# Kernel tuning notes

Hardware: AMD Instinct MI355X
Metric: run time of the kernel (lower is better)

## Reference

```python
import jax, jax.numpy as jnp
import numpy as np

LOG_2PI = float(np.log(2.0 * np.pi))


def setup_inputs() -> dict:
    key = jax.random.key(0)
    ks = jax.random.split(key, 6)
    T, K, Dx, Dy = 131072, 32, 16, 16
    X = jax.random.normal(ks[0], (T, Dx), dtype=jnp.float32)
    Y = jax.random.normal(ks[1], (T, Dy), dtype=jnp.float32)
    init_logits = jnp.zeros((K,), dtype=jnp.float32)
    W = jax.random.normal(ks[2], (K, K, Dx), dtype=jnp.float32) * 0.1
    b = jax.random.normal(ks[3], (K, K), dtype=jnp.float32) * 0.1
    mu = jax.random.normal(ks[4], (K, Dy), dtype=jnp.float32) * 0.1
    raw_log_var = jnp.zeros((K, Dy), dtype=jnp.float32)
    return {"X": X, "Y": Y, "init_logits": init_logits, "W": W, "b": b,
            "mu": mu, "raw_log_var": raw_log_var}


def _hmm_loglik(X, Y, init_logits, W, b, mu, raw_log_var):
    D = Y.shape[-1]
    # Emission log-probs for all t, k at once: [T, K]
    log_var = jnp.clip(raw_log_var, -6.0, 6.0)            # [K, Dy]
    diff = Y[:, None, :] - mu[None, :, :]                 # [T, K, Dy]
    quad = jnp.sum(diff * diff * jnp.exp(-log_var), axis=-1)  # [T, K]
    log_em = -0.5 * (D * LOG_2PI + jnp.sum(log_var, axis=-1) + quad)  # [T, K]
    # Time-varying log transition matrices, rows (axis i->j, softmax over j): [T, K, K]
    logits = b[None, :, :] + jnp.einsum('ijd,td->tij', W, X)
    log_A = jax.nn.log_softmax(logits, axis=2)
    # Forward recursion in log domain via scan.
    alpha0 = jax.nn.log_softmax(init_logits) + log_em[0]  # [K]
    def step(alpha, inp):
        lA, le = inp  # [K, K], [K]
        alpha = le + jax.scipy.special.logsumexp(alpha[:, None] + lA, axis=0)
        return alpha, None
    alphaT, _ = jax.lax.scan(step, alpha0, (log_A[1:], log_em[1:]))
    return jax.scipy.special.logsumexp(alphaT)


def reference(X, Y, init_logits, W, b, mu, raw_log_var):
    return _hmm_loglik(X, Y, init_logits, W, b, mu, raw_log_var)
```

## Files before the change

kernel.cpp:

```cpp
#include <hip/hip_runtime.h>

typedef float  f32x16 __attribute__((ext_vector_type(16)));
typedef float  f32x2  __attribute__((ext_vector_type(2)));
typedef short  short8 __attribute__((ext_vector_type(8)));
typedef unsigned short u16;
typedef unsigned int   u32;

#define LOG2PI_F 1.8378770664093453f

__device__ __forceinline__ u16 f2bf(float f) {
  u32 u = __builtin_bit_cast(u32, f);
  u32 r = (u + 0x7FFFu + ((u >> 16) & 1u)) >> 16;
  return (u16)r;
}

__global__ __launch_bounds__(256) void emis_kernel(
    const float* __restrict__ Y, const float* __restrict__ mu,
    const float* __restrict__ rlv, int T,
    float* __restrict__ E, float* __restrict__ Spart)
{
  int j  = threadIdx.x & 31;
  int ts = threadIdx.x >> 5;

  float muv[16], iv[16];
  float slv = 0.f;
  const float4* mp = (const float4*)(mu  + (size_t)j * 16);
  const float4* rp = (const float4*)(rlv + (size_t)j * 16);
#pragma unroll
  for (int q = 0; q < 4; ++q) {
    float4 m4 = mp[q], r4 = rp[q];
    float mm[4] = {m4.x, m4.y, m4.z, m4.w};
    float rr[4] = {r4.x, r4.y, r4.z, r4.w};
#pragma unroll
    for (int e = 0; e < 4; ++e) {
      float lv = fminf(fmaxf(rr[e], -6.f), 6.f);
      muv[4*q+e] = mm[e];
      iv[4*q+e]  = __expf(-lv);
      slv += lv;
    }
  }
  float base_c = 16.f * LOG2PI_F + slv;

  float sacc = 0.f;
  for (int p2 = 0; p2 < 8; ++p2) {
    int t = blockIdx.x * 64 + p2 * 8 + ts;
    if (t < T) {
      float quad = 0.f;
      const float4* yp = (const float4*)(Y + (size_t)t * 16);
#pragma unroll
      for (int q = 0; q < 4; ++q) {
        float4 y4 = yp[q];
        float yy[4] = {y4.x, y4.y, y4.z, y4.w};
#pragma unroll
        for (int e = 0; e < 4; ++e) {
          float d = yy[e] - muv[4*q+e];
          quad = fmaf(d * d, iv[4*q+e], quad);
        }
      }
      float lem = -0.5f * (base_c + quad);
      float mx = lem;
#pragma unroll
      for (int m = 16; m >= 1; m >>= 1) mx = fmaxf(mx, __shfl_xor(mx, m, 32));
      E[(size_t)t * 32 + j] = __expf(lem - mx);
      if (j == 0) sacc += mx;
    }
  }
  __shared__ float sred[8];
  if (j == 0) sred[ts] = sacc;
  __syncthreads();
  if (threadIdx.x == 0) {
    float s = 0.f;
#pragma unroll
    for (int k = 0; k < 8; ++k) s += sred[k];
    Spart[blockIdx.x] = s;
  }
}

__global__ __launch_bounds__(256) void prep_kernel(
    const float* __restrict__ W, const float* __restrict__ b,
    u16* __restrict__ Wfrag, float* __restrict__ bprime)
{
  const float INVLN2 = 1.4426950408889634f;
  int idx = blockIdx.x * 256 + threadIdx.x;
  if (idx < 16384) {
    int i = idx >> 9, rem = idx & 511, l = rem >> 3, e = rem & 7;
    int j = l & 31, h = l >> 5;
    Wfrag[idx] = f2bf(W[i * 512 + j * 16 + h * 8 + e] * INVLN2);
  }
  if (idx < 1024) bprime[idx] = b[idx] * INVLN2;
}

__device__ __forceinline__ void acc_to_bops(const f32x16& acc, uint4& B1, uint4& B2) {
  u32 pk[8];
#pragma unroll
  for (int q = 0; q < 8; ++q) {
    u32 r;
    asm("v_cvt_pk_bf16_f32 %0, %1, %2" : "=v"(r) : "v"(acc[2*q]), "v"(acc[2*q+1]));
    pk[q] = r;
  }
  asm("v_permlane32_swap_b32 %0, %1" : "+v"(pk[0]), "+v"(pk[2]));
  asm("v_permlane32_swap_b32 %0, %1" : "+v"(pk[1]), "+v"(pk[3]));
  B1 = make_uint4(pk[0], pk[1], pk[2], pk[3]);
  asm("v_permlane32_swap_b32 %0, %1" : "+v"(pk[4]), "+v"(pk[6]));
  asm("v_permlane32_swap_b32 %0, %1" : "+v"(pk[5]), "+v"(pk[7]));
  B2 = make_uint4(pk[4], pk[5], pk[6], pk[7]);
}

__device__ __forceinline__ void renorm(f32x16& acc, float& Eacc) {
  float m0 = fmaxf(fmaxf(fmaxf(acc[0], acc[1]),  fmaxf(acc[2], acc[3])),
                   fmaxf(fmaxf(acc[4], acc[5]),  fmaxf(acc[6], acc[7])));
  float m1 = fmaxf(fmaxf(fmaxf(acc[8], acc[9]),  fmaxf(acc[10], acc[11])),
                   fmaxf(fmaxf(acc[12], acc[13]), fmaxf(acc[14], acc[15])));
  float m = fmaxf(m0, m1);
#pragma unroll
  for (int off = 32; off >= 1; off >>= 1) m = fmaxf(m, __shfl_xor(m, off, 64));
  u32 be = (__builtin_bit_cast(u32, m) >> 23) & 0xFFu;
  float sc = __builtin_bit_cast(float, (253u - be) << 23);
  Eacc += (float)((int)be - 126);
#pragma unroll
  for (int r = 0; r < 16; ++r) acc[r] *= sc;
}

__device__ __forceinline__ uint4 fp8x8_to_bf16x8(uint2 c) {
  f32x2 l0 = __builtin_amdgcn_cvt_pk_f32_fp8((int)c.x, false);
  f32x2 h0 = __builtin_amdgcn_cvt_pk_f32_fp8((int)c.x, true);
  f32x2 l1 = __builtin_amdgcn_cvt_pk_f32_fp8((int)c.y, false);
  f32x2 h1 = __builtin_amdgcn_cvt_pk_f32_fp8((int)c.y, true);
  u32 w0, w1, w2, w3;
  asm("v_cvt_pk_bf16_f32 %0, %1, %2" : "=v"(w0) : "v"(l0.x), "v"(l0.y));
  asm("v_cvt_pk_bf16_f32 %0, %1, %2" : "=v"(w1) : "v"(h0.x), "v"(h0.y));
  asm("v_cvt_pk_bf16_f32 %0, %1, %2" : "=v"(w2) : "v"(l1.x), "v"(l1.y));
  asm("v_cvt_pk_bf16_f32 %0, %1, %2" : "=v"(w3) : "v"(h1.x), "v"(h1.y));
  return make_uint4(w0, w1, w2, w3);
}

__device__ __forceinline__ void bmat2_batch_fp8(
    const short8* wf, int ib0, short8 xf, const float* __restrict__ bprime,
    int h, const float* ee, int tglob, u32* q )
{
  f32x16 a[4];
#pragma unroll
  for (int e = 0; e < 4; ++e) {
    f32x16 c;
#pragma unroll
    for (int qd = 0; qd < 4; ++qd) {
      float4 b4 = *(const float4*)(bprime + (ib0 + e) * 32 + 4 * h + 8 * qd);
      c[4*qd+0] = b4.x; c[4*qd+1] = b4.y; c[4*qd+2] = b4.z; c[4*qd+3] = b4.w;
    }
    a[e] = __builtin_amdgcn_mfma_f32_32x32x16_bf16(wf[e], xf, c, 0, 0, 0);
  }
#pragma unroll
  for (int e = 0; e < 4; ++e) {
#pragma unroll
    for (int r = 0; r < 16; ++r) a[e][r] = __builtin_amdgcn_exp2f(a[e][r]);
    float s = (((a[e][0] + a[e][1]) + (a[e][2] + a[e][3])) +
               ((a[e][4] + a[e][5]) + (a[e][6] + a[e][7]))) +
              (((a[e][8] + a[e][9]) + (a[e][10] + a[e][11])) +
               ((a[e][12] + a[e][13]) + (a[e][14] + a[e][15])));
    float s2 = s, s3 = s;
    asm("v_permlane32_swap_b32 %0, %1" : "+v"(s2), "+v"(s3));
    float rv = __builtin_amdgcn_rcpf(s2 + s3);
#pragma unroll
    for (int r = 0; r < 16; ++r) a[e][r] *= rv;
  }
#pragma unroll
  for (int r = 0; r < 16; ++r) {
    float e0 = a[0][r] * ee[r], e1 = a[1][r] * ee[r];
    float e2 = a[2][r] * ee[r], e3 = a[3][r] * ee[r];
    if (tglob == 0) {
      int j = 4 * h + 8 * (r >> 2) + (r & 3);
      e0 = (ib0 + 0 == j) ? 128.f : 0.f;
      e1 = (ib0 + 1 == j) ? 128.f : 0.f;
      e2 = (ib0 + 2 == j) ? 128.f : 0.f;
      e3 = (ib0 + 3 == j) ? 128.f : 0.f;
    }
    u32 v = (u32)__builtin_amdgcn_cvt_pk_fp8_f32(e0, e1, 0, false);
    v = (u32)__builtin_amdgcn_cvt_pk_fp8_f32(e2, e3, (int)v, true);
    q[r] = v;
  }
}

__global__ __launch_bounds__(64) void fused1w_kernel(
    const float* __restrict__ X, const float* __restrict__ E,
    const u16* __restrict__ Wfrag, const float* __restrict__ bprime,
    int T, u16* __restrict__ Sg, float* __restrict__ Eg)
{
  __shared__ __align__(16) uint2 lds8[4096];
  int l = threadIdx.x, tc = l & 31, h = l >> 5;

  short8 wf[32];
#pragma unroll
  for (int it = 0; it < 32; ++it)
    wf[it] = *(const short8*)(Wfrag + ((size_t)it * 64 + l) * 8);

  f32x16 acc, zero16;
#pragma unroll
  for (int r = 0; r < 16; ++r) {
    int row = (r & 3) + 8 * (r >> 2) + 4 * h;
    acc[r]  = (row == tc) ? 1.f : 0.f;
    zero16[r] = 0.f;
  }
  float Eacc = 0.f;

  for (int grp = 0; grp < 2; ++grp) {
    int tglob = blockIdx.x * 64 + grp * 32 + tc;

    float4 xa = *(const float4*)(X + (size_t)tglob * 16 + 8 * h);
    float4 xb = *(const float4*)(X + (size_t)tglob * 16 + 8 * h + 4);
    u32 xp0, xp1, xp2, xp3;
    asm("v_cvt_pk_bf16_f32 %0, %1, %2" : "=v"(xp0) : "v"(xa.x), "v"(xa.y));
    asm("v_cvt_pk_bf16_f32 %0, %1, %2" : "=v"(xp1) : "v"(xa.z), "v"(xa.w));
    asm("v_cvt_pk_bf16_f32 %0, %1, %2" : "=v"(xp2) : "v"(xb.x), "v"(xb.y));
    asm("v_cvt_pk_bf16_f32 %0, %1, %2" : "=v"(xp3) : "v"(xb.z), "v"(xb.w));
    uint4 xu = make_uint4(xp0, xp1, xp2, xp3);
    short8 xf = __builtin_bit_cast(short8, xu);

    float ee[16];
#pragma unroll
    for (int qd = 0; qd < 4; ++qd) {
      float4 eq = *(const float4*)(E + (size_t)tglob * 32 + 4 * h + 8 * qd);
      ee[4*qd+0] = eq.x * 128.f; ee[4*qd+1] = eq.y * 128.f;
      ee[4*qd+2] = eq.z * 128.f; ee[4*qd+3] = eq.w * 128.f;
    }

#pragma unroll
    for (int b = 0; b < 4; ++b) {
      u32 q1[16], q2[16];
      bmat2_batch_fp8(wf + 8*b,     8*b,     xf, bprime, h, ee, tglob, q1);
      bmat2_batch_fp8(wf + 8*b + 4, 8*b + 4, xf, bprime, h, ee, tglob, q2);
#pragma unroll
      for (int r = 0; r < 16; ++r) {
        int j = 4*h + 8*(r>>2) + (r&3);
        int c = (j + 32 * (b & 1)) * 2 + (b >> 1);
        lds8[tc * 128 + (c ^ (tc & 15))] = make_uint2(q1[r], q2[r]);
      }
    }
    __syncthreads();

#pragma unroll 4
    for (int k = 0; k < 32; ++k) {
      int s = k & 15;
      uint2 c0 = lds8[k * 128 + ((2 * l)     ^ s)];
      uint2 c1 = lds8[k * 128 + ((2 * l + 1) ^ s)];
      uint4 A1u = fp8x8_to_bf16x8(c0);
      uint4 A2u = fp8x8_to_bf16x8(c1);
      uint4 B1, B2;
      acc_to_bops(acc, B1, B2);
      f32x16 t1 = __builtin_amdgcn_mfma_f32_32x32x16_bf16(
          __builtin_bit_cast(short8, A1u), __builtin_bit_cast(short8, B1), zero16, 0, 0, 0);
      acc = __builtin_amdgcn_mfma_f32_32x32x16_bf16(
          __builtin_bit_cast(short8, A2u), __builtin_bit_cast(short8, B2), t1, 0, 0, 0);
      if ((k & 7) == 7) renorm(acc, Eacc);
    }
    __syncthreads();
  }

  int col = l & 31;
#pragma unroll
  for (int r = 0; r < 16; ++r) {
    int row = (r & 3) + 8 * (r >> 2) + 4 * h;
    int flat = (row + 32 * ((col >> 3) & 1)) * 16 + ((col >> 4) << 3) + (col & 7);
    Sg[(size_t)blockIdx.x * 1024 + flat] = f2bf(acc[r]);
  }
  if (l == 0) Eg[blockIdx.x] = Eacc;
}

__global__ void chain_kernel(
    const uint4* __restrict__ in_frags, const float* __restrict__ in_E,
    int nchains, int mpb, u16* __restrict__ out_frags,
    float* __restrict__ out_E, float* __restrict__ out_final)
{
  int w = threadIdx.x >> 6, l = threadIdx.x & 63;
  int cid = blockIdx.x * (blockDim.x >> 6) + w;
  if (cid >= nchains) return;

  long base = (long)cid * mpb;
  const uint4* pA = in_frags + (size_t)(2 * l) + (size_t)base * 128;
  const uint4* pB = pA + 1;

  uint4 bufA[8], bufB[8];
#pragma unroll
  for (int u = 0; u < 8; ++u) {
    bufA[u] = pA[(size_t)u * 128];
    bufB[u] = pB[(size_t)u * 128];
  }

  int col = l & 31, h = l >> 5;
  f32x16 acc, zero16;
#pragma unroll
  for (int r = 0; r < 16; ++r) {
    int row = (r & 3) + 8 * (r >> 2) + 4 * h;
    acc[r]  = (row == col) ? 1.f : 0.f;
    zero16[r] = 0.f;
  }

  float Eacc = 0.f;
  if (in_E) {
    for (int k = 0; k < mpb; ++k) Eacc += in_E[base + k];
  }

  for (int s = 0; s < mpb; s += 8) {
#pragma unroll
    for (int u = 0; u < 8; ++u) {
      uint4 B1, B2;
      acc_to_bops(acc, B1, B2);
      short8 A1 = __builtin_bit_cast(short8, bufA[u]);
      short8 A2 = __builtin_bit_cast(short8, bufB[u]);
      int nm = s + u + 8;
      if (nm < mpb) {
        bufA[u] = pA[(size_t)nm * 128];
        bufB[u] = pB[(size_t)nm * 128];
      }
      f32x16 t1 = __builtin_amdgcn_mfma_f32_32x32x16_bf16(
          A1, __builtin_bit_cast(short8, B1), zero16, 0, 0, 0);
      acc = __builtin_amdgcn_mfma_f32_32x32x16_bf16(
          A2, __builtin_bit_cast(short8, B2), t1, 0, 0, 0);
    }
    renorm(acc, Eacc);
  }

  if (out_final) {
#pragma unroll
    for (int r = 0; r < 16; ++r) {
      int row = (r & 3) + 8 * (r >> 2) + 4 * h;
      out_final[row * 32 + col] = acc[r];
    }
    if (l == 0) *out_E = Eacc;
  } else {
#pragma unroll
    for (int r = 0; r < 16; ++r) {
      int row = (r & 3) + 8 * (r >> 2) + 4 * h;
      int flat = (row + 32 * ((col >> 3) & 1)) * 16 + ((col >> 4) << 3) + (col & 7);
      out_frags[(size_t)cid * 1024 + flat] = f2bf(acc[r]);
    }
    if (l == 0) out_E[cid] = Eacc;
  }
}

__global__ __launch_bounds__(64) void finalize_kernel(
    const float* __restrict__ init_logits, const float* __restrict__ E,
    const float* __restrict__ Spart, int nSpart,
    const float* __restrict__ MT, const float* __restrict__ Egrand,
    long Tcount, float* __restrict__ out)
{
  int l = threadIdx.x;
  int j = l & 31;

  float il = init_logits[j];
  float mx = il;
#pragma unroll
  for (int m = 16; m >= 1; m >>= 1) mx = fmaxf(mx, __shfl_xor(mx, m, 32));
  float pz = __expf(il - mx);
  float sz = pz;
#pragma unroll
  for (int m = 16; m >= 1; m >>= 1) sz += __shfl_xor(sz, m, 32);
  float a0 = (pz / sz) * E[j];

  float rbuf[32];
  const float4* rowp = (const float4*)(MT + j * 32);
#pragma unroll
  for (int q = 0; q < 8; ++q) {
    float4 v = rowp[q];
    rbuf[4*q+0] = v.x; rbuf[4*q+1] = v.y; rbuf[4*q+2] = v.z; rbuf[4*q+3] = v.w;
  }
  float af = 0.f;
#pragma unroll
  for (int m = 0; m < 32; ++m) af = fmaf(__shfl(a0, m, 32), rbuf[m], af);

  float sa = af;
#pragma unroll
  for (int m = 16; m >= 1; m >>= 1) sa += __shfl_xor(sa, m, 32);

  double ss = 0.0;
  for (int idx = l; idx < nSpart; idx += 64) ss += (double)Spart[idx];
#pragma unroll
  for (int m = 32; m >= 1; m >>= 1) ss += __shfl_xor(ss, m, 64);

  if (l == 0) {
    double eg = (double)(*Egrand) - 7.0 * (double)Tcount;
    double r = log((double)sa) + ss + 0.6931471805599453 * eg;
    out[0] = (float)r;
  }
}

extern "C" void kernel_launch(void* const* d_in, const int* in_sizes, int n_in,
                              void* d_out, int out_size, void* d_ws, size_t ws_size,
                              hipStream_t stream) {
  const float* X   = (const float*)d_in[0];
  const float* Y   = (const float*)d_in[1];
  const float* il  = (const float*)d_in[2];
  const float* W   = (const float*)d_in[3];
  const float* b   = (const float*)d_in[4];
  const float* mu  = (const float*)d_in[5];
  const float* rlv = (const float*)d_in[6];
  float* out = (float*)d_out;

  int T   = in_sizes[0] / 16;
  int NB0 = (T + 63) / 64;
  int NC  = T / 64;

  char* ws = (char*)d_ws;
  size_t off = 0;
  auto alloc = [&](size_t bytes) -> void* {
    void* p = ws + off;
    off = (off + bytes + 255) & ~(size_t)255;
    return p;
  };
  float* E      = (float*)alloc((size_t)T * 32 * 4);
  float* Spart  = (float*)alloc((size_t)NB0 * 4);
  u16*   Sg     = (u16*)  alloc((size_t)NC * 2048);
  float* Eg     = (float*)alloc((size_t)NC * 4);
  u16*   Rf     = (u16*)  alloc((size_t)64 * 2048);
  float* ER     = (float*)alloc((size_t)64 * 4);
  float* MT     = (float*)alloc(4096);
  float* Egrand = (float*)alloc(256);
  u16*   Wfrag  = (u16*)  alloc((size_t)16384 * 2);
  float* bprime = (float*)alloc((size_t)1024 * 4);

  prep_kernel<<<64, 256, 0, stream>>>(W, b, Wfrag, bprime);
  emis_kernel<<<NB0, 256, 0, stream>>>(Y, mu, rlv, T, E, Spart);

  fused1w_kernel<<<NC, 64, 0, stream>>>(X, E, Wfrag, bprime, T, Sg, Eg);

  chain_kernel<<<16, 256, 0, stream>>>((const uint4*)Sg, Eg, 64, NC / 64, Rf, ER, nullptr);
  chain_kernel<<<1, 64, 0, stream>>>((const uint4*)Rf, ER, 1, 64, nullptr, Egrand, MT);

  finalize_kernel<<<1, 64, 0, stream>>>(il, E, Spart, NB0, MT, Egrand, (long)T, out);
}
```

Baseline: 127.6 us.

## Fuse prep into emission kernel, merge final chain with finalize, rebalance chunk sizes

Folds the weight-prep work into the first 64 blocks of the emission kernel and merges the last chain reduction with the finalize step into one tail kernel, which removes two launches. The per-block span in the fused transition kernel grows from 64 to 128 timesteps, and the middle chain level switches to 32 matrices per chain across 32 chains. This trims launch overhead and serial steps on the critical path, but it leaves fewer blocks in the fused kernel and makes each block's serial chain twice as long. The tail kernel computes the final row-vector product directly instead of materialising a full matrix.

```diff
diff --git a/kernel.cpp b/kernel.cpp
--- a/kernel.cpp
+++ b/kernel.cpp
@@ -17,7 +17,9 @@
 __global__ __launch_bounds__(256) void emis_kernel(
     const float* __restrict__ Y, const float* __restrict__ mu,
     const float* __restrict__ rlv, int T,
-    float* __restrict__ E, float* __restrict__ Spart)
+    float* __restrict__ E, float* __restrict__ Spart,
+    const float* __restrict__ W, const float* __restrict__ b,
+    u16* __restrict__ Wfrag, float* __restrict__ bprime)
 {
   int j  = threadIdx.x & 31;
   int ts = threadIdx.x >> 5;
@@ -74,20 +76,17 @@
     for (int k = 0; k < 8; ++k) s += sred[k];
     Spart[blockIdx.x] = s;
   }
-}
-
-__global__ __launch_bounds__(256) void prep_kernel(
-    const float* __restrict__ W, const float* __restrict__ b,
-    u16* __restrict__ Wfrag, float* __restrict__ bprime)
-{
-  const float INVLN2 = 1.4426950408889634f;
-  int idx = blockIdx.x * 256 + threadIdx.x;
-  if (idx < 16384) {
-    int i = idx >> 9, rem = idx & 511, l = rem >> 3, e = rem & 7;
-    int j = l & 31, h = l >> 5;
-    Wfrag[idx] = f2bf(W[i * 512 + j * 16 + h * 8 + e] * INVLN2);
-  }
-  if (idx < 1024) bprime[idx] = b[idx] * INVLN2;
+
+  if (blockIdx.x < 64) {
+    const float INVLN2 = 1.4426950408889634f;
+    int idx = blockIdx.x * 256 + threadIdx.x;
+    {
+      int i = idx >> 9, rem = idx & 511, l = rem >> 3, e = rem & 7;
+      int jj = l & 31, h = l >> 5;
+      Wfrag[idx] = f2bf(W[i * 512 + jj * 16 + h * 8 + e] * INVLN2);
+    }
+    if (idx < 1024) bprime[idx] = b[idx] * INVLN2;
+  }
 }
 
 __device__ __forceinline__ void acc_to_bops(const f32x16& acc, uint4& B1, uint4& B2) {
@@ -202,8 +201,8 @@
   }
   float Eacc = 0.f;
 
-  for (int grp = 0; grp < 2; ++grp) {
-    int tglob = blockIdx.x * 64 + grp * 32 + tc;
+  for (int grp = 0; grp < 4; ++grp) {
+    int tglob = blockIdx.x * 128 + grp * 32 + tc;
 
     float4 xa = *(const float4*)(X + (size_t)tglob * 16 + 8 * h);
     float4 xb = *(const float4*)(X + (size_t)tglob * 16 + 8 * h + 4);
@@ -268,7 +267,7 @@
 __global__ void chain_kernel(
     const uint4* __restrict__ in_frags, const float* __restrict__ in_E,
     int nchains, int mpb, u16* __restrict__ out_frags,
-    float* __restrict__ out_E, float* __restrict__ out_final)
+    float* __restrict__ out_E)
 {
   int w = threadIdx.x >> 6, l = threadIdx.x & 63;
   int cid = blockIdx.x * (blockDim.x >> 6) + w;
@@ -319,57 +318,85 @@
     renorm(acc, Eacc);
   }
 
-  if (out_final) {
-#pragma unroll
-    for (int r = 0; r < 16; ++r) {
-      int row = (r & 3) + 8 * (r >> 2) + 4 * h;
-      out_final[row * 32 + col] = acc[r];
-    }
-    if (l == 0) *out_E = Eacc;
-  } else {
-#pragma unroll
-    for (int r = 0; r < 16; ++r) {
-      int row = (r & 3) + 8 * (r >> 2) + 4 * h;
-      int flat = (row + 32 * ((col >> 3) & 1)) * 16 + ((col >> 4) << 3) + (col & 7);
-      out_frags[(size_t)cid * 1024 + flat] = f2bf(acc[r]);
-    }
-    if (l == 0) out_E[cid] = Eacc;
-  }
-}
-
-__global__ __launch_bounds__(64) void finalize_kernel(
+#pragma unroll
+  for (int r = 0; r < 16; ++r) {
+    int row = (r & 3) + 8 * (r >> 2) + 4 * h;
+    int flat = (row + 32 * ((col >> 3) & 1)) * 16 + ((col >> 4) << 3) + (col & 7);
+    out_frags[(size_t)cid * 1024 + flat] = f2bf(acc[r]);
+  }
+  if (l == 0) out_E[cid] = Eacc;
+}
+
+__global__ __launch_bounds__(64) void tail_kernel(
+    const uint4* __restrict__ Rf, const float* __restrict__ ER, int mpb,
     const float* __restrict__ init_logits, const float* __restrict__ E,
-    const float* __restrict__ Spart, int nSpart,
-    const float* __restrict__ MT, const float* __restrict__ Egrand,
-    long Tcount, float* __restrict__ out)
+    const float* __restrict__ Spart, int nSpart, long Tcount,
+    float* __restrict__ out)
 {
-  int l = threadIdx.x;
-  int j = l & 31;
-
-  float il = init_logits[j];
-  float mx = il;
-#pragma unroll
-  for (int m = 16; m >= 1; m >>= 1) mx = fmaxf(mx, __shfl_xor(mx, m, 32));
-  float pz = __expf(il - mx);
-  float sz = pz;
-#pragma unroll
-  for (int m = 16; m >= 1; m >>= 1) sz += __shfl_xor(sz, m, 32);
-  float a0 = (pz / sz) * E[j];
-
-  float rbuf[32];
-  const float4* rowp = (const float4*)(MT + j * 32);
-#pragma unroll
-  for (int q = 0; q < 8; ++q) {
-    float4 v = rowp[q];
-    rbuf[4*q+0] = v.x; rbuf[4*q+1] = v.y; rbuf[4*q+2] = v.z; rbuf[4*q+3] = v.w;
-  }
-  float af = 0.f;
-#pragma unroll
-  for (int m = 0; m < 32; ++m) af = fmaf(__shfl(a0, m, 32), rbuf[m], af);
-
-  float sa = af;
-#pragma unroll
-  for (int m = 16; m >= 1; m >>= 1) sa += __shfl_xor(sa, m, 32);
+  int l = threadIdx.x, col = l & 31, h = l >> 5;
+
+  __shared__ float a0s[32];
+  {
+    float il = init_logits[col];
+    float mx = il;
+#pragma unroll
+    for (int m = 16; m >= 1; m >>= 1) mx = fmaxf(mx, __shfl_xor(mx, m, 32));
+    float pz = __expf(il - mx);
+    float sz = pz;
+#pragma unroll
+    for (int m = 16; m >= 1; m >>= 1) sz += __shfl_xor(sz, m, 32);
+    if (l < 32) a0s[l] = (pz / sz) * E[l];
+  }
+  __syncthreads();
+
+  const uint4* pA = Rf + (size_t)(2 * l);
+  const uint4* pB = pA + 1;
+  uint4 bufA[8], bufB[8];
+#pragma unroll
+  for (int u = 0; u < 8; ++u) {
+    bufA[u] = pA[(size_t)u * 128];
+    bufB[u] = pB[(size_t)u * 128];
+  }
+
+  f32x16 acc, zero16;
+#pragma unroll
+  for (int r = 0; r < 16; ++r) {
+    int row = (r & 3) + 8 * (r >> 2) + 4 * h;
+    acc[r]  = (row == col) ? 1.f : 0.f;
+    zero16[r] = 0.f;
+  }
+
+  float Eacc = 0.f;
+  for (int k = 0; k < mpb; ++k) Eacc += ER[k];
+
+  for (int s = 0; s < mpb; s += 8) {
+#pragma unroll
+    for (int u = 0; u < 8; ++u) {
+      uint4 B1, B2;
+      acc_to_bops(acc, B1, B2);
+      short8 A1 = __builtin_bit_cast(short8, bufA[u]);
+      short8 A2 = __builtin_bit_cast(short8, bufB[u]);
+      int nm = s + u + 8;
+      if (nm < mpb) {
+        bufA[u] = pA[(size_t)nm * 128];
+        bufB[u] = pB[(size_t)nm * 128];
+      }
+      f32x16 t1 = __builtin_amdgcn_mfma_f32_32x32x16_bf16(
+          A1, __builtin_bit_cast(short8, B1), zero16, 0, 0, 0);
+      acc = __builtin_amdgcn_mfma_f32_32x32x16_bf16(
+          A2, __builtin_bit_cast(short8, B2), t1, 0, 0, 0);
+    }
+    renorm(acc, Eacc);
+  }
+
+  float partial = 0.f;
+#pragma unroll
+  for (int r = 0; r < 16; ++r) {
+    int row = (r & 3) + 8 * (r >> 2) + 4 * h;
+    partial = fmaf(a0s[row], acc[r], partial);
+  }
+#pragma unroll
+  for (int off = 32; off >= 1; off >>= 1) partial += __shfl_xor(partial, off, 64);
 
   double ss = 0.0;
   for (int idx = l; idx < nSpart; idx += 64) ss += (double)Spart[idx];
@@ -377,8 +404,8 @@
   for (int m = 32; m >= 1; m >>= 1) ss += __shfl_xor(ss, m, 64);
 
   if (l == 0) {
-    double eg = (double)(*Egrand) - 7.0 * (double)Tcount;
-    double r = log((double)sa) + ss + 0.6931471805599453 * eg;
+    double eg = (double)Eacc - 7.0 * (double)Tcount;
+    double r = log((double)partial) + ss + 0.6931471805599453 * eg;
     out[0] = (float)r;
   }
 }
@@ -397,7 +424,7 @@
 
   int T   = in_sizes[0] / 16;
   int NB0 = (T + 63) / 64;
-  int NC  = T / 64;
+  int NC  = T / 128;
 
   char* ws = (char*)d_ws;
   size_t off = 0;
@@ -412,18 +439,16 @@
   float* Eg     = (float*)alloc((size_t)NC * 4);
   u16*   Rf     = (u16*)  alloc((size_t)64 * 2048);
   float* ER     = (float*)alloc((size_t)64 * 4);
-  float* MT     = (float*)alloc(4096);
-  float* Egrand = (float*)alloc(256);
   u16*   Wfrag  = (u16*)  alloc((size_t)16384 * 2);
   float* bprime = (float*)alloc((size_t)1024 * 4);
 
-  prep_kernel<<<64, 256, 0, stream>>>(W, b, Wfrag, bprime);
-  emis_kernel<<<NB0, 256, 0, stream>>>(Y, mu, rlv, T, E, Spart);
+  emis_kernel<<<NB0, 256, 0, stream>>>(Y, mu, rlv, T, E, Spart, W, b, Wfrag, bprime);
 
   fused1w_kernel<<<NC, 64, 0, stream>>>(X, E, Wfrag, bprime, T, Sg, Eg);
 
-  chain_kernel<<<16, 256, 0, stream>>>((const uint4*)Sg, Eg, 64, NC / 64, Rf, ER, nullptr);
-  chain_kernel<<<1, 64, 0, stream>>>((const uint4*)Rf, ER, 1, 64, nullptr, Egrand, MT);
-
-  finalize_kernel<<<1, 64, 0, stream>>>(il, E, Spart, NB0, MT, Egrand, (long)T, out);
-}
+  int nch2 = NC / 32;
+  chain_kernel<<<(nch2 + 3) / 4, 256, 0, stream>>>((const uint4*)Sg, Eg, nch2, 32, Rf, ER);
+
+  tail_kernel<<<1, 64, 0, stream>>>((const uint4*)Rf, ER, nch2, il, E, Spart, NB0,
+                                    (long)T, out);
+}
```

After: 117.9 us. -7.6%, faster.
